# Kernel optimization log

Hardware: AMD Instinct MI355X
Metric: run time of the kernel (lower is better)

Reference implementation:

```python
import jax, jax.numpy as jnp
import numpy as np

MEMORY_SIZE = 8192
FEATURE_DIM = 512
NUM_QUERIES = 32768
EPS = 1e-12  # guard for sqrt in cdist


def setup_inputs() -> dict:
    key = jax.random.key(0)
    k1, k2, k3, k4 = jax.random.split(key, 4)
    return {
        "features": jax.random.normal(k1, (MEMORY_SIZE, FEATURE_DIM), dtype=jnp.float32),
        "positions": jax.random.normal(k2, (MEMORY_SIZE, 3), dtype=jnp.float32),
        "query_positions": jax.random.normal(k3, (NUM_QUERIES, 3), dtype=jnp.float32),
        "position_embeddings": jax.random.normal(k4, (MEMORY_SIZE, 3), dtype=jnp.float32),
    }


def _cdist(a, b):
    # Euclidean distance via ||a||^2 + ||b||^2 - 2 a.b; avoids [Q,M,3] intermediate.
    a2 = jnp.sum(a * a, axis=-1, keepdims=True)          # [Q,1]
    b2 = jnp.sum(b * b, axis=-1, keepdims=True).T        # [1,M]
    d2 = a2 + b2 - 2.0 * (a @ b.T)                       # [Q,M]
    return jnp.sqrt(jnp.maximum(d2, EPS))


def reference(features, positions, query_positions, position_embeddings):
    # --- update ---
    positions_norm = positions / jnp.linalg.norm(positions, axis=-1, keepdims=True)
    embeddings_norm = position_embeddings / jnp.linalg.norm(position_embeddings, axis=-1, keepdims=True)
    sim = positions_norm @ embeddings_norm.T             # [M,M]
    attn = jax.nn.softmax(sim, axis=-1)
    memory = attn @ features                              # [M,F]
    new_pos_emb = attn @ positions                        # [M,3]
    # --- query ---
    dist = _cdist(query_positions, new_pos_emb)           # [Q,M]
    qattn = jax.nn.softmax(-dist, axis=-1)
    retrieved = qattn @ memory                            # [Q,F]
    return retrieved
```

## Files before the change

### kernel.cpp

```cpp
#include <hip/hip_runtime.h>
#include <stdint.h>
#include <stddef.h>

#define M_SZ 8192
#define F_DIM 512
#define N_Q 32768

typedef __attribute__((ext_vector_type(4))) float f32x4;
typedef __attribute__((ext_vector_type(8))) __bf16 bf16x8;
typedef __attribute__((ext_vector_type(2))) __bf16 bf16x2;

__device__ __forceinline__ float bits_to_f(unsigned u) {
    union { unsigned u; float f; } v; v.u = u; return v.f;
}
__device__ __forceinline__ unsigned pk_bf16(float a, float b) {
    union { bf16x2 v; unsigned u; } cv;
    cv.v.x = (__bf16)a; cv.v.y = (__bf16)b;
    return cv.u;
}
__device__ __forceinline__ unsigned short f2bf(float x) {
    union { bf16x2 v; unsigned u; } cv;
    cv.v.x = (__bf16)x; cv.v.y = (__bf16)0.0f;
    return (unsigned short)(cv.u & 0xffffu);
}
__device__ __forceinline__ bf16x8 as_bf16x8(uint4 u) {
    union { uint4 a; bf16x8 b; } cv; cv.a = u; return cv.b;
}

__global__ void prep_kernel(const float* __restrict__ pos,
                            const float* __restrict__ emb,
                            float* __restrict__ pn4,
                            float* __restrict__ en4,
                            float* __restrict__ pos4) {
    int i = blockIdx.x * 256 + threadIdx.x;
    if (i >= M_SZ) return;
    float x = pos[i * 3 + 0], y = pos[i * 3 + 1], z = pos[i * 3 + 2];
    float inv = 1.0f / __builtin_amdgcn_sqrtf(x * x + y * y + z * z);
    pn4[i * 4 + 0] = x * inv; pn4[i * 4 + 1] = y * inv;
    pn4[i * 4 + 2] = z * inv; pn4[i * 4 + 3] = 0.0f;
    pos4[i * 4 + 0] = x; pos4[i * 4 + 1] = y;
    pos4[i * 4 + 2] = z; pos4[i * 4 + 3] = 0.0f;
    float ex = emb[i * 3 + 0], ey = emb[i * 3 + 1], ez = emb[i * 3 + 2];
    float einv = 1.0f / __builtin_amdgcn_sqrtf(ex * ex + ey * ey + ez * ez);
    en4[i * 4 + 0] = ex * einv; en4[i * 4 + 1] = ey * einv;
    en4[i * 4 + 2] = ez * einv; en4[i * 4 + 3] = 0.0f;
}

__global__ void transpose_kernel(const float* __restrict__ feat,
                                 unsigned short* __restrict__ featT) {
    __shared__ float tile[64 * 65];
    const int jb = blockIdx.x * 64, fb = blockIdx.y * 64;
    const int t = threadIdx.x;
#pragma unroll
    for (int p = 0; p < 16; ++p) {
        int idx = p * 256 + t;
        int j = idx >> 6, f = idx & 63;
        tile[j * 65 + f] = feat[(size_t)(jb + j) * F_DIM + fb + f];
    }
    __syncthreads();
#pragma unroll
    for (int p = 0; p < 16; ++p) {
        int idx = p * 256 + t;
        int f = idx >> 6, j = idx & 63;
        featT[(size_t)(fb + f) * M_SZ + jb + j] = f2bf(tile[j * 65 + f]);
    }
}

__launch_bounds__(512, 2)
__global__ void build_memory_kernel(const float* __restrict__ pn4,
                                    const float* __restrict__ en4,
                                    const float* __restrict__ pos4,
                                    const unsigned short* __restrict__ featT,
                                    unsigned short* __restrict__ memT,
                                    float* __restrict__ npe4) {
    constexpr int BM = 128, BK = 64, PSTR = BK + 8;
    __shared__ unsigned short pbuf[2][BM * PSTR];
    __shared__ f32x4 red4[512];
    __shared__ float lbuf[BM];

    const int t = threadIdx.x;
    const int lane = t & 63, wv = t >> 6;
    const int col = lane & 15, quad = lane >> 4;
    const int bid = blockIdx.x;
    const int fb = bid & 3;
    const int mb = (bid >> 2) * BM;
    const int r = t & 127, jq = t >> 7;

    const f32x4 pnr = ((const f32x4*)pn4)[mb + r];
    const f32x4* en = (const f32x4*)en4;
    const f32x4* ps = (const f32x4*)pos4;

    const unsigned short* bp =
        featT + (size_t)(fb * 128 + wv * 16 + col) * M_SZ + quad * 8;

    f32x4 acc[8];
    const f32x4 zero4 = {0.f, 0.f, 0.f, 0.f};
#pragma unroll
    for (int m = 0; m < 8; ++m) acc[m] = zero4;
    float nx = 0.f, ny = 0.f, nz = 0.f, lp = 0.f;

    uint4 h0A, h0B, h1v;
    h0A = *(const uint4*)(bp);

#define B_COMP(JB, SIDE)                                                     \
    {                                                                        \
        _Pragma("unroll") for (int hh = 0; hh < 2; ++hh) {                   \
            unsigned us[4];                                                  \
            _Pragma("unroll") for (int i = 0; i < 8; i += 2) {               \
                int j = (JB) + jq * 16 + hh * 8 + i;                         \
                f32x4 e0 = en[j], e1 = en[j + 1];                            \
                f32x4 p0 = ps[j], p1 = ps[j + 1];                            \
                float s0 = fmaf(pnr.x, e0.x, fmaf(pnr.y, e0.y, pnr.z * e0.z)); \
                float s1 = fmaf(pnr.x, e1.x, fmaf(pnr.y, e1.y, pnr.z * e1.z)); \
                float w0 = __builtin_amdgcn_exp2f(s0 * 1.44269504f);         \
                float w1 = __builtin_amdgcn_exp2f(s1 * 1.44269504f);         \
                unsigned u = pk_bf16(w0, w1);                                \
                float w0r = bits_to_f(u << 16), w1r = bits_to_f(u & 0xffff0000u); \
                lp += w0r + w1r;                                             \
                nx = fmaf(w0r, p0.x, fmaf(w1r, p1.x, nx));                   \
                ny = fmaf(w0r, p0.y, fmaf(w1r, p1.y, ny));                   \
                nz = fmaf(w0r, p0.z, fmaf(w1r, p1.z, nz));                   \
                us[i >> 1] = u;                                              \
            }                                                                \
            *(uint4*)(&pbuf[(SIDE)][r * PSTR + jq * 16 + hh * 8]) =          \
                make_uint4(us[0], us[1], us[2], us[3]);                      \
        }                                                                    \
    }

#define B_MFMA(SIDE, VB0, VB1)                                               \
    {                                                                        \
        _Pragma("unroll") for (int m = 0; m < 8; ++m) {                      \
            bf16x8 a = *(const bf16x8*)(&pbuf[(SIDE)][(m * 16 + col) * PSTR + quad * 8]); \
            acc[m] = __builtin_amdgcn_mfma_f32_16x16x32_bf16(                \
                a, as_bf16x8(VB0), acc[m], 0, 0, 0);                         \
        }                                                                    \
        _Pragma("unroll") for (int m = 0; m < 8; ++m) {                      \
            bf16x8 a = *(const bf16x8*)(&pbuf[(SIDE)][(m * 16 + col) * PSTR + 32 + quad * 8]); \
            acc[m] = __builtin_amdgcn_mfma_f32_16x16x32_bf16(                \
                a, as_bf16x8(VB1), acc[m], 0, 0, 0);                         \
        }                                                                    \
    }

#define B_BODY(CURH0, NXTH0, SIDE, JNXT)                                     \
    {                                                                        \
        h1v = *(const uint4*)(bp + 32);                                      \
        NXTH0 = *(const uint4*)(bp + 64);                                    \
        bp += 64;                                                            \
        B_COMP(JNXT, (SIDE) ^ 1)                                             \
        B_MFMA(SIDE, CURH0, h1v)                                             \
        __syncthreads();                                                     \
    }

    B_COMP(0, 0)
    __syncthreads();

    int jn = BK;
    for (int kt = 0; kt < 126; kt += 2) {
        B_BODY(h0A, h0B, 0, jn) jn += BK;
        B_BODY(h0B, h0A, 1, jn) jn += BK;
    }
    B_BODY(h0A, h0B, 0, jn)
    {
        h1v = *(const uint4*)(bp + 32);
        B_MFMA(1, h0B, h1v)
    }
#undef B_BODY
#undef B_MFMA
#undef B_COMP

    f32x4 mine = {nx, ny, nz, lp};
    red4[t] = mine;
    __syncthreads();
    if (t < BM) {
        f32x4 s = red4[t];
#pragma unroll
        for (int g = 1; g < 4; ++g) {
            f32x4 o = red4[t + 128 * g];
            s.x += o.x; s.y += o.y; s.z += o.z; s.w += o.w;
        }
        lbuf[t] = s.w;
        if (fb == 0) {
            float inv = 1.0f / s.w;
            float X = s.x * inv, Y = s.y * inv, Z = s.z * inv;
            f32x4 o = {X, Y, Z, X * X + Y * Y + Z * Z};
            ((f32x4*)npe4)[mb + t] = o;
        }
    }
    __syncthreads();

    {
        int fg = fb * 128 + wv * 16 + col;
#pragma unroll
        for (int m = 0; m < 8; ++m) {
            f32x4 l4 = *(const f32x4*)(lbuf + m * 16 + quad * 4);
            f32x4 inv4 = {1.0f / l4.x, 1.0f / l4.y, 1.0f / l4.z, 1.0f / l4.w};
            int mg = mb + m * 16 + quad * 4;
            uint2 o;
            o.x = pk_bf16(acc[m].x * inv4.x, acc[m].y * inv4.y);
            o.y = pk_bf16(acc[m].z * inv4.z, acc[m].w * inv4.w);
            *(uint2*)(memT + (size_t)fg * M_SZ + mg) = o;
        }
    }
}

__launch_bounds__(512, 2)
__global__ void query_kernel(const float* __restrict__ qpos,
                             const float* __restrict__ npe4,
                             const unsigned short* __restrict__ memT,
                             float* __restrict__ out) {
    constexpr int BM = 128, BK = 64, PSTR = BK + 8;
    __shared__ unsigned short pbuf[2][BM * PSTR];
    __shared__ float redl[512];
    __shared__ float lbuf[BM];

    const int t = threadIdx.x;
    const int lane = t & 63, wv = t >> 6;
    const int col = lane & 15, quad = lane >> 4;
    const int qb = blockIdx.x * BM;
    const int r = t & 127, jq = t >> 7;

    const float qx = qpos[(size_t)(qb + r) * 3 + 0];
    const float qy = qpos[(size_t)(qb + r) * 3 + 1];
    const float qz = qpos[(size_t)(qb + r) * 3 + 2];
    const float q2 = qx * qx + qy * qy + qz * qz;
    const float m2x = -2.0f * qx, m2y = -2.0f * qy, m2z = -2.0f * qz;

    const f32x4* nsrc = (const f32x4*)npe4;

    const unsigned short* bp[4];
#pragma unroll
    for (int n = 0; n < 4; ++n)
        bp[n] = memT + (size_t)(wv * 64 + n * 16 + col) * M_SZ + quad * 8;

    f32x4 acc[8][4];
    const f32x4 zero4 = {0.f, 0.f, 0.f, 0.f};
#pragma unroll
    for (int m = 0; m < 8; ++m)
#pragma unroll
        for (int n = 0; n < 4; ++n) acc[m][n] = zero4;
    float lp = 0.f;

    uint4 h0A[4], h0B[4], h1[4];
#pragma unroll
    for (int n = 0; n < 4; ++n) h0A[n] = *(const uint4*)(bp[n]);

#define Q_COMP(JB, SIDE)                                                     \
    {                                                                        \
        _Pragma("unroll") for (int hh = 0; hh < 2; ++hh) {                   \
            unsigned us[4];                                                  \
            _Pragma("unroll") for (int i = 0; i < 8; i += 2) {               \
                int j = (JB) + jq * 16 + hh * 8 + i;                         \
                f32x4 n0 = nsrc[j], n1 = nsrc[j + 1];                        \
                float s0 = fmaf(m2x, n0.x, fmaf(m2y, n0.y, fmaf(m2z, n0.z, q2 + n0.w))); \
                float s1 = fmaf(m2x, n1.x, fmaf(m2y, n1.y, fmaf(m2z, n1.z, q2 + n1.w))); \
                s0 = fmaxf(s0, 1e-12f); s1 = fmaxf(s1, 1e-12f);              \
                float w0 = __builtin_amdgcn_exp2f(__builtin_amdgcn_sqrtf(s0) * -1.44269504f); \
                float w1 = __builtin_amdgcn_exp2f(__builtin_amdgcn_sqrtf(s1) * -1.44269504f); \
                unsigned u = pk_bf16(w0, w1);                                \
                lp += bits_to_f(u << 16) + bits_to_f(u & 0xffff0000u);       \
                us[i >> 1] = u;                                              \
            }                                                                \
            *(uint4*)(&pbuf[(SIDE)][r * PSTR + jq * 16 + hh * 8]) =          \
                make_uint4(us[0], us[1], us[2], us[3]);                      \
        }                                                                    \
    }

#define Q_MFMA(SIDE, VB0, VB1)                                               \
    {                                                                        \
        _Pragma("unroll") for (int m = 0; m < 8; ++m) {                      \
            bf16x8 a = *(const bf16x8*)(&pbuf[(SIDE)][(m * 16 + col) * PSTR + quad * 8]); \
            _Pragma("unroll") for (int n = 0; n < 4; ++n)                    \
                acc[m][n] = __builtin_amdgcn_mfma_f32_16x16x32_bf16(         \
                    a, as_bf16x8(VB0[n]), acc[m][n], 0, 0, 0);               \
        }                                                                    \
        _Pragma("unroll") for (int m = 0; m < 8; ++m) {                      \
            bf16x8 a = *(const bf16x8*)(&pbuf[(SIDE)][(m * 16 + col) * PSTR + 32 + quad * 8]); \
            _Pragma("unroll") for (int n = 0; n < 4; ++n)                    \
                acc[m][n] = __builtin_amdgcn_mfma_f32_16x16x32_bf16(         \
                    a, as_bf16x8(VB1[n]), acc[m][n], 0, 0, 0);               \
        }                                                                    \
    }

#define Q_BODY(CURH0, NXTH0, SIDE, JNXT)                                     \
    {                                                                        \
        _Pragma("unroll") for (int n = 0; n < 4; ++n)                        \
            h1[n] = *(const uint4*)(bp[n] + 32);                             \
        _Pragma("unroll") for (int n = 0; n < 4; ++n) {                      \
            NXTH0[n] = *(const uint4*)(bp[n] + 64);                          \
            bp[n] += 64;                                                     \
        }                                                                    \
        Q_COMP(JNXT, (SIDE) ^ 1)                                             \
        Q_MFMA(SIDE, CURH0, h1)                                              \
        __syncthreads();                                                     \
    }

    Q_COMP(0, 0)
    __syncthreads();

    int jn = BK;
    for (int kt = 0; kt < 126; kt += 2) {
        Q_BODY(h0A, h0B, 0, jn) jn += BK;
        Q_BODY(h0B, h0A, 1, jn) jn += BK;
    }
    Q_BODY(h0A, h0B, 0, jn)
    {
#pragma unroll
        for (int n = 0; n < 4; ++n) h1[n] = *(const uint4*)(bp[n] + 32);
        Q_MFMA(1, h0B, h1)
    }
#undef Q_BODY
#undef Q_MFMA
#undef Q_COMP

    redl[t] = lp;
    __syncthreads();
    if (t < BM) lbuf[t] = redl[t] + redl[t + 128] + redl[t + 256] + redl[t + 384];
    __syncthreads();

#pragma unroll
    for (int m = 0; m < 8; ++m) {
        f32x4 l4 = *(const f32x4*)(lbuf + m * 16 + quad * 4);
        f32x4 inv4 = {1.0f / l4.x, 1.0f / l4.y, 1.0f / l4.z, 1.0f / l4.w};
        int qg = qb + m * 16 + quad * 4;
#pragma unroll
        for (int n = 0; n < 4; ++n) {
            int fg = wv * 64 + n * 16 + col;
            out[(size_t)(qg + 0) * F_DIM + fg] = acc[m][n].x * inv4.x;
            out[(size_t)(qg + 1) * F_DIM + fg] = acc[m][n].y * inv4.y;
            out[(size_t)(qg + 2) * F_DIM + fg] = acc[m][n].z * inv4.z;
            out[(size_t)(qg + 3) * F_DIM + fg] = acc[m][n].w * inv4.w;
        }
    }
}

extern "C" void kernel_launch(void* const* d_in, const int* in_sizes, int n_in,
                              void* d_out, int out_size, void* d_ws, size_t ws_size,
                              hipStream_t stream) {
    const float* features  = (const float*)d_in[0];
    const float* positions = (const float*)d_in[1];
    const float* qpos      = (const float*)d_in[2];
    const float* pemb      = (const float*)d_in[3];
    float* out = (float*)d_out;
    char* ws = (char*)d_ws;

    unsigned short* featT = (unsigned short*)(ws);
    unsigned short* memT  = (unsigned short*)(ws + 8388608);
    float* npe4 = (float*)(ws + 16777216);
    float* pn4  = (float*)(ws + 16908288);
    float* en4  = (float*)(ws + 17039360);
    float* pos4 = (float*)(ws + 17170432);

    hipLaunchKernelGGL(prep_kernel, dim3(M_SZ / 256), dim3(256), 0, stream,
                       positions, pemb, pn4, en4, pos4);
    hipLaunchKernelGGL(transpose_kernel, dim3(M_SZ / 64, F_DIM / 64), dim3(256), 0, stream,
                       features, featT);
    hipLaunchKernelGGL(build_memory_kernel, dim3((M_SZ / 128) * 4), dim3(512), 0, stream,
                       pn4, en4, pos4, featT, memT, npe4);
    hipLaunchKernelGGL(query_kernel, dim3(N_Q / 128), dim3(512), 0, stream,
                       qpos, npe4, memT, out);
}
```

Before: 887.4 us.

## Halve query K-tile to 32 and use lighter LDS-only workgroup barrier

Cuts the query kernel's K-step from 64 to 32, so each iteration generates a smaller probability tile and runs half as many MFMAs. This doubles the iteration count but shrinks LDS and register footprint (one B register set per stage instead of two). It also replaces __syncthreads with a custom barrier that waits only on LDS counters plus a sched_barrier, so outstanding global loads need not drain at each sync. The cost is more barriers per unit of work and a scheduling fence that may limit how the compiler interleaves instructions.

```diff
diff --git a/kernel.cpp b/kernel.cpp
--- a/kernel.cpp
+++ b/kernel.cpp
@@ -25,6 +25,12 @@
 }
 __device__ __forceinline__ bf16x8 as_bf16x8(uint4 u) {
     union { uint4 a; bf16x8 b; } cv; cv.a = u; return cv.b;
+}
+
+__device__ __forceinline__ void wg_barrier() {
+    asm volatile("s_waitcnt lgkmcnt(0)" ::: "memory");
+    __builtin_amdgcn_s_barrier();
+    __builtin_amdgcn_sched_barrier(0);
 }
 
 __global__ void prep_kernel(const float* __restrict__ pos,
@@ -148,11 +154,11 @@
         bp += 64;                                                            \
         B_COMP(JNXT, (SIDE) ^ 1)                                             \
         B_MFMA(SIDE, CURH0, h1v)                                             \
-        __syncthreads();                                                     \
+        wg_barrier();                                                        \
     }
 
     B_COMP(0, 0)
-    __syncthreads();
+    wg_barrier();
 
     int jn = BK;
     for (int kt = 0; kt < 126; kt += 2) {
@@ -208,7 +214,7 @@
                              const float* __restrict__ npe4,
                              const unsigned short* __restrict__ memT,
                              float* __restrict__ out) {
-    constexpr int BM = 128, BK = 64, PSTR = BK + 8;
+    constexpr int BM = 128, BK = 32, PSTR = BK + 8;
     __shared__ unsigned short pbuf[2][BM * PSTR];
     __shared__ float redl[512];
     __shared__ float lbuf[BM];
@@ -240,77 +246,63 @@
         for (int n = 0; n < 4; ++n) acc[m][n] = zero4;
     float lp = 0.f;
 
-    uint4 h0A[4], h0B[4], h1[4];
-#pragma unroll
-    for (int n = 0; n < 4; ++n) h0A[n] = *(const uint4*)(bp[n]);
-
-#define Q_COMP(JB, SIDE)                                                     \
-    {                                                                        \
-        _Pragma("unroll") for (int hh = 0; hh < 2; ++hh) {                   \
-            unsigned us[4];                                                  \
-            _Pragma("unroll") for (int i = 0; i < 8; i += 2) {               \
-                int j = (JB) + jq * 16 + hh * 8 + i;                         \
-                f32x4 n0 = nsrc[j], n1 = nsrc[j + 1];                        \
-                float s0 = fmaf(m2x, n0.x, fmaf(m2y, n0.y, fmaf(m2z, n0.z, q2 + n0.w))); \
-                float s1 = fmaf(m2x, n1.x, fmaf(m2y, n1.y, fmaf(m2z, n1.z, q2 + n1.w))); \
-                s0 = fmaxf(s0, 1e-12f); s1 = fmaxf(s1, 1e-12f);              \
-                float w0 = __builtin_amdgcn_exp2f(__builtin_amdgcn_sqrtf(s0) * -1.44269504f); \
-                float w1 = __builtin_amdgcn_exp2f(__builtin_amdgcn_sqrtf(s1) * -1.44269504f); \
-                unsigned u = pk_bf16(w0, w1);                                \
-                lp += bits_to_f(u << 16) + bits_to_f(u & 0xffff0000u);       \
-                us[i >> 1] = u;                                              \
-            }                                                                \
-            *(uint4*)(&pbuf[(SIDE)][r * PSTR + jq * 16 + hh * 8]) =          \
-                make_uint4(us[0], us[1], us[2], us[3]);                      \
-        }                                                                    \
-    }
-
-#define Q_MFMA(SIDE, VB0, VB1)                                               \
+    uint4 vbA[4], vbB[4];
+#pragma unroll
+    for (int n = 0; n < 4; ++n) vbA[n] = *(const uint4*)(bp[n]);
+
+#define Q_GEN_P(JB, SIDE)                                                    \
+    {                                                                        \
+        unsigned pk4[4];                                                     \
+        _Pragma("unroll") for (int i = 0; i < 8; i += 2) {                   \
+            int j = (JB) + jq * 8 + i;                                       \
+            f32x4 n0 = nsrc[j], n1 = nsrc[j + 1];                            \
+            float s0 = fmaf(m2x, n0.x, fmaf(m2y, n0.y, fmaf(m2z, n0.z, q2 + n0.w))); \
+            float s1 = fmaf(m2x, n1.x, fmaf(m2y, n1.y, fmaf(m2z, n1.z, q2 + n1.w))); \
+            s0 = fmaxf(s0, 1e-12f); s1 = fmaxf(s1, 1e-12f);                  \
+            float w0 = __builtin_amdgcn_exp2f(__builtin_amdgcn_sqrtf(s0) * -1.44269504f); \
+            float w1 = __builtin_amdgcn_exp2f(__builtin_amdgcn_sqrtf(s1) * -1.44269504f); \
+            unsigned u = pk_bf16(w0, w1);                                    \
+            lp += bits_to_f(u << 16) + bits_to_f(u & 0xffff0000u);           \
+            pk4[i >> 1] = u;                                                 \
+        }                                                                    \
+        *(uint4*)(&pbuf[SIDE][r * PSTR + jq * 8]) =                          \
+            make_uint4(pk4[0], pk4[1], pk4[2], pk4[3]);                      \
+    }
+
+#define Q_MFMA(VB, SIDE)                                                     \
     {                                                                        \
         _Pragma("unroll") for (int m = 0; m < 8; ++m) {                      \
-            bf16x8 a = *(const bf16x8*)(&pbuf[(SIDE)][(m * 16 + col) * PSTR + quad * 8]); \
+            bf16x8 a = *(const bf16x8*)(&pbuf[SIDE][(m * 16 + col) * PSTR + quad * 8]); \
             _Pragma("unroll") for (int n = 0; n < 4; ++n)                    \
                 acc[m][n] = __builtin_amdgcn_mfma_f32_16x16x32_bf16(         \
-                    a, as_bf16x8(VB0[n]), acc[m][n], 0, 0, 0);               \
-        }                                                                    \
-        _Pragma("unroll") for (int m = 0; m < 8; ++m) {                      \
-            bf16x8 a = *(const bf16x8*)(&pbuf[(SIDE)][(m * 16 + col) * PSTR + 32 + quad * 8]); \
-            _Pragma("unroll") for (int n = 0; n < 4; ++n)                    \
-                acc[m][n] = __builtin_amdgcn_mfma_f32_16x16x32_bf16(         \
-                    a, as_bf16x8(VB1[n]), acc[m][n], 0, 0, 0);               \
-        }                                                                    \
-    }
-
-#define Q_BODY(CURH0, NXTH0, SIDE, JNXT)                                     \
-    {                                                                        \
-        _Pragma("unroll") for (int n = 0; n < 4; ++n)                        \
-            h1[n] = *(const uint4*)(bp[n] + 32);                             \
+                    a, as_bf16x8(VB[n]), acc[m][n], 0, 0, 0);                \
+        }                                                                    \
+    }
+
+#define Q_BODY(CUR, NXT, SIDE, JNXT)                                         \
+    {                                                                        \
         _Pragma("unroll") for (int n = 0; n < 4; ++n) {                      \
-            NXTH0[n] = *(const uint4*)(bp[n] + 64);                          \
-            bp[n] += 64;                                                     \
-        }                                                                    \
-        Q_COMP(JNXT, (SIDE) ^ 1)                                             \
-        Q_MFMA(SIDE, CURH0, h1)                                              \
-        __syncthreads();                                                     \
-    }
-
-    Q_COMP(0, 0)
-    __syncthreads();
+            NXT[n] = *(const uint4*)(bp[n] + BK);                            \
+            bp[n] += BK;                                                     \
+        }                                                                    \
+        Q_GEN_P(JNXT, SIDE ^ 1)                                              \
+        Q_MFMA(CUR, SIDE)                                                    \
+        wg_barrier();                                                        \
+    }
+
+    Q_GEN_P(0, 0)
+    wg_barrier();
 
     int jn = BK;
-    for (int kt = 0; kt < 126; kt += 2) {
-        Q_BODY(h0A, h0B, 0, jn) jn += BK;
-        Q_BODY(h0B, h0A, 1, jn) jn += BK;
-    }
-    Q_BODY(h0A, h0B, 0, jn)
-    {
-#pragma unroll
-        for (int n = 0; n < 4; ++n) h1[n] = *(const uint4*)(bp[n] + 32);
-        Q_MFMA(1, h0B, h1)
-    }
+    for (int kt = 0; kt < 254; kt += 2) {
+        Q_BODY(vbA, vbB, 0, jn) jn += BK;
+        Q_BODY(vbB, vbA, 1, jn) jn += BK;
+    }
+    Q_BODY(vbA, vbB, 0, jn)
+    Q_MFMA(vbB, 1)
 #undef Q_BODY
 #undef Q_MFMA
-#undef Q_COMP
+#undef Q_GEN_P
 
     redl[t] = lp;
     __syncthreads();
```

New measurement: 845.2 us. -4.8%, faster.
